# Optimization experiments

Hardware: AMD Instinct MI355X
Metric: run time of the kernel (lower is better)

The kernel has to match this reference:

```python
import jax, jax.numpy as jnp
import numpy as np

N_HEADS = 8
HEAD_D = 64


def setup_inputs() -> dict:
    key = jax.random.key(0)
    ks = jax.random.split(key, 7)
    b, ds, dc = 4, 4096, 256
    ls, lc = 512, 512
    inner = N_HEADS * HEAD_D  # 512
    out_dim = 512
    data = jax.random.normal(ks[0], (b, ds, dc), dtype=jnp.float32)
    latent = jax.random.normal(ks[1], (b, ls, lc), dtype=jnp.float32)
    # torch nn.Linear weights are [out_features, in_features]
    Wq = jax.random.normal(ks[2], (inner, lc), dtype=jnp.float32) * (lc ** -0.5)
    Wk = jax.random.normal(ks[3], (inner, dc), dtype=jnp.float32) * (dc ** -0.5)
    Wv = jax.random.normal(ks[4], (inner, dc), dtype=jnp.float32) * (dc ** -0.5)
    Wo = jax.random.normal(ks[5], (out_dim, inner), dtype=jnp.float32) * (inner ** -0.5)
    bo = jax.random.normal(ks[6], (out_dim,), dtype=jnp.float32) * 0.02
    return {"data": data, "latent": latent, "Wq": Wq, "Wk": Wk, "Wv": Wv, "Wo": Wo, "bo": bo}


def reference(data, latent, Wq, Wk, Wv, Wo, bo):
    b, ds, _ = data.shape
    ls = latent.shape[1]
    scale = HEAD_D ** -0.5
    # projections, split into heads
    Q = (latent @ Wq.T).reshape(b, ls, N_HEADS, HEAD_D)  # [b,ls,h,d]
    K = (data @ Wk.T).reshape(b, ds, N_HEADS, HEAD_D)    # [b,ds,h,d]
    V = (data @ Wv.T).reshape(b, ds, N_HEADS, HEAD_D)
    # logits [b, ds, ls, h]; original broadcasts then sums over head_d -> einsum
    logits = jnp.einsum('blhd,bshd->bslh', Q, K) * scale
    # softmax over key axis (dim 1 = ds), matching attn_logits.softmax(1)
    attn = jax.nn.softmax(logits, axis=1)
    # weighted sum over keys: [b, ls, h, d] -> [b, ls, inner]
    out = jnp.einsum('bshd,bslh->blhd', V, attn).reshape(b, ls, N_HEADS * HEAD_D)
    # output Linear (dropout is identity in eval)
    return out @ Wo.T + bo
```

## Files before the change

kernel.cpp:

```cpp
#include <hip/hip_runtime.h>

typedef __bf16 bf16;
typedef __bf16 bf16x4 __attribute__((ext_vector_type(4)));
typedef __bf16 bf16x8 __attribute__((ext_vector_type(8)));
typedef float  f32x4  __attribute__((ext_vector_type(4)));


__device__ __forceinline__ bf16x8 cvt8(float4 a, float4 b) {
    bf16x8 r;
    r[0] = (bf16)a.x; r[1] = (bf16)a.y; r[2] = (bf16)a.z; r[3] = (bf16)a.w;
    r[4] = (bf16)b.x; r[5] = (bf16)b.y; r[6] = (bf16)b.z; r[7] = (bf16)b.w;
    return r;
}

#define LDT 136
__global__ __launch_bounds__(256) void proj_kvq(
    const float* __restrict__ data, const float* __restrict__ latent,
    const float* __restrict__ Wk, const float* __restrict__ Wv, const float* __restrict__ Wq,
    bf16* __restrict__ K_b, bf16* __restrict__ Vt_b, bf16* __restrict__ Q_b)
{
    __shared__ __align__(16) bf16 arena[128 * LDT];

    const int bx = blockIdx.x;
    const int tid = threadIdx.x;
    const int wave = tid >> 6, lane = tid & 63;
    const int wm = wave >> 1, wn = wave & 1;
    const int l15 = lane & 15, quad = lane >> 4;
    const int rowA = tid >> 2;
    const int c8 = (tid & 3) * 8;

    if (bx >= 64) {
        const int t = bx - 64;
        const int m0 = (t & 127) * 128, n0 = (t >> 7) * 128;
        bf16* As  = arena;
        bf16* Bks = arena + 4096;
        bf16* Bvs = arena + 8192;

        const float* Ar0 = data + (size_t)(m0 + rowA) * 256 + c8;
        const float* Ar1 = Ar0 + 64 * 256;
        const float* Kr0 = Wk + (size_t)(n0 + rowA) * 256 + c8;
        const float* Kr1 = Kr0 + 64 * 256;
        const float* Vr0 = Wv + (size_t)(n0 + rowA) * 256 + c8;
        const float* Vr1 = Vr0 + 64 * 256;

        f32x4 accK[4][4] = {}, accV[4][4] = {};
        float4 a00,a01,a10,a11, k00,k01,k10,k11, v00,v01,v10,v11;

#define LOADF(k) do { \
        a00 = *(const float4*)(Ar0 + (k)); a01 = *(const float4*)(Ar0 + (k) + 4); \
        a10 = *(const float4*)(Ar1 + (k)); a11 = *(const float4*)(Ar1 + (k) + 4); \
        k00 = *(const float4*)(Kr0 + (k)); k01 = *(const float4*)(Kr0 + (k) + 4); \
        k10 = *(const float4*)(Kr1 + (k)); k11 = *(const float4*)(Kr1 + (k) + 4); \
        v00 = *(const float4*)(Vr0 + (k)); v01 = *(const float4*)(Vr0 + (k) + 4); \
        v10 = *(const float4*)(Vr1 + (k)); v11 = *(const float4*)(Vr1 + (k) + 4); \
    } while (0)

        LOADF(0);
        for (int k0 = 0; k0 < 256; k0 += 32) {
            __syncthreads();
            *(bf16x8*)(As + (size_t)tid * 8)         = cvt8(a00, a01);
            *(bf16x8*)(As + 2048 + (size_t)tid * 8)  = cvt8(a10, a11);
            *(bf16x8*)(Bks + (size_t)tid * 8)        = cvt8(k00, k01);
            *(bf16x8*)(Bks + 2048 + (size_t)tid * 8) = cvt8(k10, k11);
            *(bf16x8*)(Bvs + (size_t)tid * 8)        = cvt8(v00, v01);
            *(bf16x8*)(Bvs + 2048 + (size_t)tid * 8) = cvt8(v10, v11);
            if (k0 + 32 < 256) LOADF(k0 + 32);
            __syncthreads();

            bf16x8 af[4];
            #pragma unroll
            for (int mt = 0; mt < 4; mt++)
                af[mt] = *(const bf16x8*)(As + (wm * 64 + mt * 16 + l15) * 32 + quad * 8);
            #pragma unroll
            for (int nt = 0; nt < 4; nt++) {
                bf16x8 bk = *(const bf16x8*)(Bks + (wn * 64 + nt * 16 + l15) * 32 + quad * 8);
                #pragma unroll
                for (int mt = 0; mt < 4; mt++)
                    accK[mt][nt] = __builtin_amdgcn_mfma_f32_16x16x32_bf16(af[mt], bk, accK[mt][nt], 0, 0, 0);
            }
            #pragma unroll
            for (int nt = 0; nt < 4; nt++) {
                bf16x8 bv = *(const bf16x8*)(Bvs + (wn * 64 + nt * 16 + l15) * 32 + quad * 8);
                #pragma unroll
                for (int mt = 0; mt < 4; mt++)
                    accV[mt][nt] = __builtin_amdgcn_mfma_f32_16x16x32_bf16(af[mt], bv, accV[mt][nt], 0, 0, 0);
            }
        }
#undef LOADF

        __syncthreads();
        #pragma unroll
        for (int mt = 0; mt < 4; mt++)
            #pragma unroll
            for (int nt = 0; nt < 4; nt++)
                #pragma unroll
                for (int r = 0; r < 4; r++) {
                    int ml = wm * 64 + mt * 16 + quad * 4 + r;
                    int nl = wn * 64 + nt * 16 + l15;
                    arena[ml * LDT + nl] = (bf16)accK[mt][nt][r];
                }
        __syncthreads();
        #pragma unroll
        for (int c = 0; c < 8; c++) {
            int idx = c * 256 + tid;
            int row = idx >> 4, col = (idx & 15) * 8;
            bf16x8 vv = *(const bf16x8*)(arena + row * LDT + col);
            int m = m0 + row, n = n0 + col;
            *(bf16x8*)(K_b + (size_t)((m >> 12) * 8 + (n >> 6)) * 262144 + (m & 4095) * 64 + (n & 63)) = vv;
        }
        __syncthreads();
        #pragma unroll
        for (int mt = 0; mt < 4; mt++)
            #pragma unroll
            for (int nt = 0; nt < 4; nt++)
                #pragma unroll
                for (int r = 0; r < 4; r++) {
                    int ml = wm * 64 + mt * 16 + quad * 4 + r;
                    int nl = wn * 64 + nt * 16 + l15;
                    arena[nl * LDT + ml] = (bf16)accV[mt][nt][r];
                }
        __syncthreads();
        #pragma unroll
        for (int c = 0; c < 8; c++) {
            int idx = c * 256 + tid;
            int row = idx >> 4, col = (idx & 15) * 8;
            bf16x8 vv = *(const bf16x8*)(arena + row * LDT + col);
            int d = n0 + row, s = m0 + col;
            *(bf16x8*)(Vt_b + (size_t)((s >> 12) * 8 + (d >> 6)) * 262144 + (d & 63) * 4096 + (s & 4095)) = vv;
        }
    } else {
        const int m0 = (bx & 15) * 128, n0 = (bx >> 4) * 128;
        bf16* As = arena;
        bf16* Bs = arena + 4096;

        const float* Ar0 = latent + (size_t)(m0 + rowA) * 512 + c8;
        const float* Ar1 = Ar0 + 64 * 512;
        const float* Br0 = Wq + (size_t)(n0 + rowA) * 512 + c8;
        const float* Br1 = Br0 + 64 * 512;

        f32x4 acc[4][4] = {};
        float4 a00, a01, a10, a11, b00, b01, b10, b11;

#define LOADQ(k) do { \
        a00 = *(const float4*)(Ar0 + (k));  a01 = *(const float4*)(Ar0 + (k) + 4); \
        a10 = *(const float4*)(Ar1 + (k));  a11 = *(const float4*)(Ar1 + (k) + 4); \
        b00 = *(const float4*)(Br0 + (k));  b01 = *(const float4*)(Br0 + (k) + 4); \
        b10 = *(const float4*)(Br1 + (k));  b11 = *(const float4*)(Br1 + (k) + 4); \
    } while (0)

        LOADQ(0);
        for (int k0 = 0; k0 < 512; k0 += 32) {
            __syncthreads();
            *(bf16x8*)(As + (size_t)tid * 8)        = cvt8(a00, a01);
            *(bf16x8*)(As + 2048 + (size_t)tid * 8) = cvt8(a10, a11);
            *(bf16x8*)(Bs + (size_t)tid * 8)        = cvt8(b00, b01);
            *(bf16x8*)(Bs + 2048 + (size_t)tid * 8) = cvt8(b10, b11);
            if (k0 + 32 < 512) LOADQ(k0 + 32);
            __syncthreads();

            bf16x8 af[4], bfr[4];
            #pragma unroll
            for (int mt = 0; mt < 4; mt++)
                af[mt] = *(const bf16x8*)(As + (wm * 64 + mt * 16 + l15) * 32 + quad * 8);
            #pragma unroll
            for (int nt = 0; nt < 4; nt++)
                bfr[nt] = *(const bf16x8*)(Bs + (wn * 64 + nt * 16 + l15) * 32 + quad * 8);
            #pragma unroll
            for (int mt = 0; mt < 4; mt++)
                #pragma unroll
                for (int nt = 0; nt < 4; nt++)
                    acc[mt][nt] = __builtin_amdgcn_mfma_f32_16x16x32_bf16(af[mt], bfr[nt], acc[mt][nt], 0, 0, 0);
        }
#undef LOADQ

        __syncthreads();
        #pragma unroll
        for (int mt = 0; mt < 4; mt++)
            #pragma unroll
            for (int nt = 0; nt < 4; nt++)
                #pragma unroll
                for (int r = 0; r < 4; r++) {
                    int ml = wm * 64 + mt * 16 + quad * 4 + r;
                    int nl = wn * 64 + nt * 16 + l15;
                    arena[ml * LDT + nl] = (bf16)(acc[mt][nt][r] * 0.125f);
                }
        __syncthreads();
        #pragma unroll
        for (int c = 0; c < 8; c++) {
            int idx = c * 256 + tid;
            int row = idx >> 4, col = (idx & 15) * 8;
            bf16x8 vv = *(const bf16x8*)(arena + row * LDT + col);
            int m = m0 + row, n = n0 + col;
            *(bf16x8*)(Q_b + (size_t)((m >> 9) * 8 + (n >> 6)) * 32768 + (m & 511) * 64 + (n & 63)) = vv;
        }
    }
}

#define LDK 72
#define LDP 72
__global__ __launch_bounds__(256) void flash_attn(
    const bf16* __restrict__ Q, const bf16* __restrict__ K,
    const bf16* __restrict__ Vt, float* __restrict__ Opart, float* __restrict__ lbuf)
{
    __shared__ bf16 Ks[64 * LDK];
    __shared__ bf16 Vs[64 * LDK];
    __shared__ bf16 Ps[4][2 * 16 * LDP];

    const int tid = threadIdx.x;
    const int bx = blockIdx.x;
    const int qt = bx >> 7;
    const int bh = (bx & 127) >> 2;
    const int ks = bx & 3;
    const int wave = tid >> 6, lane = tid & 63;
    const int l15 = lane & 15, quad = lane >> 4;

    const bf16* Qb = Q + (size_t)bh * 32768 + (size_t)(qt * 128 + wave * 32 + l15) * 64;
    bf16x8 aq[2][2];
    aq[0][0] = *(const bf16x8*)(Qb + quad * 8);
    aq[0][1] = *(const bf16x8*)(Qb + 32 + quad * 8);
    aq[1][0] = *(const bf16x8*)(Qb + 1024 + quad * 8);
    aq[1][1] = *(const bf16x8*)(Qb + 1024 + 32 + quad * 8);

    const bf16* Kb = K + (size_t)bh * 262144;
    const bf16* Vb = Vt + (size_t)bh * 262144;

    f32x4 oacc[2][4] = {};
    float lsum[2] = {0.f, 0.f};

    const int i0 = tid, i1 = tid + 256;
    const int r0 = i0 >> 3, c0 = (i0 & 7) * 8;
    const int r1 = i1 >> 3, c1 = (i1 & 7) * 8;

    const int kstart = ks * 1024, kend = kstart + 1024;

    uint4 pk0 = *(const uint4*)(Kb + (size_t)(kstart + r0) * 64 + c0);
    uint4 pk1 = *(const uint4*)(Kb + (size_t)(kstart + r1) * 64 + c1);
    uint4 pv0 = *(const uint4*)(Vb + (size_t)r0 * 4096 + kstart + c0);
    uint4 pv1 = *(const uint4*)(Vb + (size_t)r1 * 4096 + kstart + c1);

    bf16* Pw = &Ps[wave][0];

    for (int key0 = kstart; key0 < kend; key0 += 64) {
        __syncthreads();
        *(uint4*)(Ks + r0 * LDK + c0) = pk0;
        *(uint4*)(Ks + r1 * LDK + c1) = pk1;
        *(uint4*)(Vs + r0 * LDK + c0) = pv0;
        *(uint4*)(Vs + r1 * LDK + c1) = pv1;
        if (key0 + 64 < kend) {
            pk0 = *(const uint4*)(Kb + (size_t)(key0 + 64 + r0) * 64 + c0);
            pk1 = *(const uint4*)(Kb + (size_t)(key0 + 64 + r1) * 64 + c1);
            pv0 = *(const uint4*)(Vb + (size_t)r0 * 4096 + key0 + 64 + c0);
            pv1 = *(const uint4*)(Vb + (size_t)r1 * 4096 + key0 + 64 + c1);
        }
        __syncthreads();

        __builtin_amdgcn_s_setprio(1);
        #pragma unroll
        for (int mt = 0; mt < 4; mt++) {
            bf16x8 bk0 = *(const bf16x8*)(Ks + (mt * 16 + l15) * LDK + quad * 8);
            bf16x8 bk1 = *(const bf16x8*)(Ks + (mt * 16 + l15) * LDK + 32 + quad * 8);
            #pragma unroll
            for (int u = 0; u < 2; u++) {
                f32x4 z = {};
                z = __builtin_amdgcn_mfma_f32_16x16x32_bf16(bk0, aq[u][0], z, 0, 0, 0);
                z = __builtin_amdgcn_mfma_f32_16x16x32_bf16(bk1, aq[u][1], z, 0, 0, 0);
                bf16x4 pv4;
                float s = 0.f;
                #pragma unroll
                for (int r = 0; r < 4; r++) {
                    float e = __expf(z[r]);
                    s += e;
                    pv4[r] = (bf16)e;
                }
                lsum[u] += s;
                *(bf16x4*)(Pw + u * 16 * LDP + l15 * LDP + mt * 16 + quad * 4) = pv4;
            }
        }
        __builtin_amdgcn_s_setprio(0);

        bf16x8 ap[2][2];
        #pragma unroll
        for (int u = 0; u < 2; u++) {
            ap[u][0] = *(const bf16x8*)(Pw + u * 16 * LDP + l15 * LDP + quad * 8);
            ap[u][1] = *(const bf16x8*)(Pw + u * 16 * LDP + l15 * LDP + 32 + quad * 8);
        }
        __builtin_amdgcn_s_setprio(1);
        #pragma unroll
        for (int dt = 0; dt < 4; dt++) {
            bf16x8 bv0 = *(const bf16x8*)(Vs + (dt * 16 + l15) * LDK + quad * 8);
            bf16x8 bv1 = *(const bf16x8*)(Vs + (dt * 16 + l15) * LDK + 32 + quad * 8);
            #pragma unroll
            for (int u = 0; u < 2; u++) {
                oacc[u][dt] = __builtin_amdgcn_mfma_f32_16x16x32_bf16(ap[u][0], bv0, oacc[u][dt], 0, 0, 0);
                oacc[u][dt] = __builtin_amdgcn_mfma_f32_16x16x32_bf16(ap[u][1], bv1, oacc[u][dt], 0, 0, 0);
            }
        }
        __builtin_amdgcn_s_setprio(0);
    }

    #pragma unroll
    for (int u = 0; u < 2; u++) {
        lsum[u] += __shfl_xor(lsum[u], 16, 64);
        lsum[u] += __shfl_xor(lsum[u], 32, 64);
    }

    #pragma unroll
    for (int u = 0; u < 2; u++) {
        const int rowbase = bh * 512 + qt * 128 + wave * 32 + u * 16 + quad * 4;
        #pragma unroll
        for (int dt = 0; dt < 4; dt++) {
            #pragma unroll
            for (int r = 0; r < 4; r++) {
                Opart[((size_t)ks * 16384 + rowbase + r) * 64 + dt * 16 + l15] = oacc[u][dt][r];
            }
        }
        if (quad == 0) {
            lbuf[(size_t)ks * 16384 + bh * 512 + qt * 128 + wave * 32 + u * 16 + l15] = lsum[u];
        }
    }
}

__global__ __launch_bounds__(256) void gemm_out(
    const float* __restrict__ Opart, const float* __restrict__ lbuf,
    const float* __restrict__ Wo, const float* __restrict__ bo, float* __restrict__ out)
{
    __shared__ bf16 As[64 * 32];
    __shared__ bf16 Bs[64 * 32];
    const int tid = threadIdx.x;
    const int m0 = blockIdx.x * 64, n0 = blockIdx.y * 64;
    const int wave = tid >> 6, lane = tid & 63;
    const int wm = wave >> 1, wn = wave & 1;
    const int l15 = lane & 15, quad = lane >> 4;
    const int rowA = tid >> 2;
    const int c8 = (tid & 3) * 8;
    const int m = m0 + rowA;
    const int mhi = (m >> 9) << 3, mlo = m & 511;

    f32x4 acc[2][2] = {};
    float4 pa[8]; float pl[4]; float4 pb0, pb1;

    auto loadA = [&](int k0) {
        int kc = k0 + c8;
        int arow = (mhi + (kc >> 6)) * 512 + mlo;
        int d0 = kc & 63;
        #pragma unroll
        for (int ks = 0; ks < 4; ks++) {
            pl[ks] = lbuf[(size_t)ks * 16384 + arow];
            pa[2 * ks]     = *(const float4*)(Opart + ((size_t)ks * 16384 + arow) * 64 + d0);
            pa[2 * ks + 1] = *(const float4*)(Opart + ((size_t)ks * 16384 + arow) * 64 + d0 + 4);
        }
    };
    auto loadB = [&](int k0) {
        pb0 = *(const float4*)(Wo + (size_t)(n0 + rowA) * 512 + k0 + c8);
        pb1 = *(const float4*)(Wo + (size_t)(n0 + rowA) * 512 + k0 + c8 + 4);
    };

    loadA(0); loadB(0);

    for (int k0 = 0; k0 < 512; k0 += 32) {
        __syncthreads();
        {
            float L = pl[0] + pl[1] + pl[2] + pl[3];
            float inv = 1.0f / L;
            float4 s0, s1;
            s0.x = pa[0].x + pa[2].x + pa[4].x + pa[6].x;
            s0.y = pa[0].y + pa[2].y + pa[4].y + pa[6].y;
            s0.z = pa[0].z + pa[2].z + pa[4].z + pa[6].z;
            s0.w = pa[0].w + pa[2].w + pa[4].w + pa[6].w;
            s1.x = pa[1].x + pa[3].x + pa[5].x + pa[7].x;
            s1.y = pa[1].y + pa[3].y + pa[5].y + pa[7].y;
            s1.z = pa[1].z + pa[3].z + pa[5].z + pa[7].z;
            s1.w = pa[1].w + pa[3].w + pa[5].w + pa[7].w;
            s0.x *= inv; s0.y *= inv; s0.z *= inv; s0.w *= inv;
            s1.x *= inv; s1.y *= inv; s1.z *= inv; s1.w *= inv;
            *(bf16x8*)(As + (size_t)tid * 8) = cvt8(s0, s1);
            *(bf16x8*)(Bs + (size_t)tid * 8) = cvt8(pb0, pb1);
        }
        if (k0 + 32 < 512) { loadA(k0 + 32); loadB(k0 + 32); }
        __syncthreads();

        bf16x8 af[2], bfr[2];
        #pragma unroll
        for (int mt = 0; mt < 2; mt++)
            af[mt] = *(const bf16x8*)(As + (wm * 32 + mt * 16 + l15) * 32 + quad * 8);
        #pragma unroll
        for (int nt = 0; nt < 2; nt++)
            bfr[nt] = *(const bf16x8*)(Bs + (wn * 32 + nt * 16 + l15) * 32 + quad * 8);
        #pragma unroll
        for (int mt = 0; mt < 2; mt++)
            #pragma unroll
            for (int nt = 0; nt < 2; nt++)
                acc[mt][nt] = __builtin_amdgcn_mfma_f32_16x16x32_bf16(af[mt], bfr[nt], acc[mt][nt], 0, 0, 0);
    }

    #pragma unroll
    for (int mt = 0; mt < 2; mt++) {
        #pragma unroll
        for (int nt = 0; nt < 2; nt++) {
            #pragma unroll
            for (int r = 0; r < 4; r++) {
                int mm = m0 + wm * 32 + mt * 16 + quad * 4 + r;
                int nn = n0 + wn * 32 + nt * 16 + l15;
                out[(size_t)mm * 512 + nn] = acc[mt][nt][r] + bo[nn];
            }
        }
    }
}

extern "C" void kernel_launch(void* const* d_in, const int* in_sizes, int n_in,
                              void* d_out, int out_size, void* d_ws, size_t ws_size,
                              hipStream_t stream) {
    const float* data   = (const float*)d_in[0];
    const float* latent = (const float*)d_in[1];
    const float* Wq = (const float*)d_in[2];
    const float* Wk = (const float*)d_in[3];
    const float* Wv = (const float*)d_in[4];
    const float* Wo = (const float*)d_in[5];
    const float* bo = (const float*)d_in[6];
    float* out = (float*)d_out;

    bf16* ws = (bf16*)d_ws;
    bf16* Q_b    = ws;
    bf16* K_b    = Q_b + 1048576;
    bf16* Vt_b   = K_b + 8388608;
    float* Opart = (float*)(Vt_b + 8388608);
    float* lbuf  = Opart + 4 * 16384 * 64;

    proj_kvq<<<576, 256, 0, stream>>>(data, latent, Wk, Wv, Wq, K_b, Vt_b, Q_b);
    flash_attn<<<512, 256, 0, stream>>>(Q_b, K_b, Vt_b, Opart, lbuf);
    gemm_out<<<dim3(32, 8), 256, 0, stream>>>(Opart, lbuf, Wo, bo, out);
}
```

Before: 149.1 us.

## Pre-convert inputs to bf16, use async global-to-LDS loads, split merge from output GEMM

Adds a kernel that converts data, latent and all weights to bf16 up front, folding the attention scale into Wq. The projection kernel then stages bf16 tiles through double-buffered direct global-to-LDS loads instead of register fp32 loads and conversion. The split-K merge of partial attention outputs moves out of the output GEMM into its own kernel that writes bf16 O. This removes redundant fp32 reloads and conversions inside the GEMMs, in exchange for two extra launches and an extra read and write pass over the data.

```diff
diff --git a/kernel.cpp b/kernel.cpp
--- a/kernel.cpp
+++ b/kernel.cpp
@@ -13,82 +13,102 @@
     return r;
 }
 
+__device__ __forceinline__ void gload16(const bf16* g, bf16* l) {
+    __builtin_amdgcn_global_load_lds(
+        (const __attribute__((address_space(1))) unsigned int*)(g),
+        (__attribute__((address_space(3))) unsigned int*)(l), 16, 0, 0);
+}
+
+__global__ __launch_bounds__(256) void cvt_in(
+    const float* __restrict__ data, const float* __restrict__ latent,
+    const float* __restrict__ Wq, const float* __restrict__ Wk,
+    const float* __restrict__ Wv, const float* __restrict__ Wo,
+    bf16* __restrict__ db, bf16* __restrict__ lb, bf16* __restrict__ qb,
+    bf16* __restrict__ kb, bf16* __restrict__ vb, bf16* __restrict__ ob)
+{
+    const int bx = blockIdx.x;
+    const float* src; bf16* dst; float scale = 1.0f; int base;
+    if      (bx < 2048) { src = data;   dst = db; base = bx; }
+    else if (bx < 2560) { src = latent; dst = lb; base = bx - 2048; }
+    else if (bx < 2688) { src = Wq;     dst = qb; base = bx - 2560; scale = 0.125f; }
+    else if (bx < 2752) { src = Wk;     dst = kb; base = bx - 2688; }
+    else if (bx < 2816) { src = Wv;     dst = vb; base = bx - 2752; }
+    else                { src = Wo;     dst = ob; base = bx - 2816; }
+    size_t off = (size_t)base * 2048 + (size_t)threadIdx.x * 8;
+    float4 a = *(const float4*)(src + off);
+    float4 b = *(const float4*)(src + off + 4);
+    a.x *= scale; a.y *= scale; a.z *= scale; a.w *= scale;
+    b.x *= scale; b.y *= scale; b.z *= scale; b.w *= scale;
+    *(bf16x8*)(dst + off) = cvt8(a, b);
+}
+
 #define LDT 136
 __global__ __launch_bounds__(256) void proj_kvq(
-    const float* __restrict__ data, const float* __restrict__ latent,
-    const float* __restrict__ Wk, const float* __restrict__ Wv, const float* __restrict__ Wq,
+    const bf16* __restrict__ data, const bf16* __restrict__ latent,
+    const bf16* __restrict__ Wk, const bf16* __restrict__ Wv, const bf16* __restrict__ Wq,
     bf16* __restrict__ K_b, bf16* __restrict__ Vt_b, bf16* __restrict__ Q_b)
 {
-    __shared__ __align__(16) bf16 arena[128 * LDT];
+    __shared__ __align__(16) bf16 arena[24576];
 
     const int bx = blockIdx.x;
     const int tid = threadIdx.x;
     const int wave = tid >> 6, lane = tid & 63;
     const int wm = wave >> 1, wn = wave & 1;
     const int l15 = lane & 15, quad = lane >> 4;
-    const int rowA = tid >> 2;
-    const int c8 = (tid & 3) * 8;
+    const int rowS = wave * 32 + (lane >> 2);
+    const int colS = (lane & 3) * 8;
 
     if (bx >= 64) {
         const int t = bx - 64;
         const int m0 = (t & 127) * 128, n0 = (t >> 7) * 128;
-        bf16* As  = arena;
-        bf16* Bks = arena + 4096;
-        bf16* Bvs = arena + 8192;
-
-        const float* Ar0 = data + (size_t)(m0 + rowA) * 256 + c8;
-        const float* Ar1 = Ar0 + 64 * 256;
-        const float* Kr0 = Wk + (size_t)(n0 + rowA) * 256 + c8;
-        const float* Kr1 = Kr0 + 64 * 256;
-        const float* Vr0 = Wv + (size_t)(n0 + rowA) * 256 + c8;
-        const float* Vr1 = Vr0 + 64 * 256;
+
+        const bf16* Asrc = data + (size_t)(m0 + rowS) * 256 + colS;
+        const bf16* Ksrc = Wk   + (size_t)(n0 + rowS) * 256 + colS;
+        const bf16* Vsrc = Wv   + (size_t)(n0 + rowS) * 256 + colS;
 
         f32x4 accK[4][4] = {}, accV[4][4] = {};
-        float4 a00,a01,a10,a11, k00,k01,k10,k11, v00,v01,v10,v11;
-
-#define LOADF(k) do { \
-        a00 = *(const float4*)(Ar0 + (k)); a01 = *(const float4*)(Ar0 + (k) + 4); \
-        a10 = *(const float4*)(Ar1 + (k)); a11 = *(const float4*)(Ar1 + (k) + 4); \
-        k00 = *(const float4*)(Kr0 + (k)); k01 = *(const float4*)(Kr0 + (k) + 4); \
-        k10 = *(const float4*)(Kr1 + (k)); k11 = *(const float4*)(Kr1 + (k) + 4); \
-        v00 = *(const float4*)(Vr0 + (k)); v01 = *(const float4*)(Vr0 + (k) + 4); \
-        v10 = *(const float4*)(Vr1 + (k)); v11 = *(const float4*)(Vr1 + (k) + 4); \
+
+#define STAGE_KV(buf, k0) do { \
+        bf16* Lb = arena + (buf) * 12288 + wave * 1024; \
+        gload16(Asrc + (k0),        Lb);          \
+        gload16(Asrc + (k0) + 4096, Lb + 512);    \
+        gload16(Ksrc + (k0),        Lb + 4096);   \
+        gload16(Ksrc + (k0) + 4096, Lb + 4608);   \
+        gload16(Vsrc + (k0),        Lb + 8192);   \
+        gload16(Vsrc + (k0) + 4096, Lb + 8704);   \
     } while (0)
 
-        LOADF(0);
+        STAGE_KV(0, 0);
+        asm volatile("s_waitcnt vmcnt(0)" ::: "memory");
+        __syncthreads();
+        int cur = 0;
         for (int k0 = 0; k0 < 256; k0 += 32) {
-            __syncthreads();
-            *(bf16x8*)(As + (size_t)tid * 8)         = cvt8(a00, a01);
-            *(bf16x8*)(As + 2048 + (size_t)tid * 8)  = cvt8(a10, a11);
-            *(bf16x8*)(Bks + (size_t)tid * 8)        = cvt8(k00, k01);
-            *(bf16x8*)(Bks + 2048 + (size_t)tid * 8) = cvt8(k10, k11);
-            *(bf16x8*)(Bvs + (size_t)tid * 8)        = cvt8(v00, v01);
-            *(bf16x8*)(Bvs + 2048 + (size_t)tid * 8) = cvt8(v10, v11);
-            if (k0 + 32 < 256) LOADF(k0 + 32);
-            __syncthreads();
+            if (k0 + 32 < 256) STAGE_KV(cur ^ 1, k0 + 32);
+            const bf16* B = arena + cur * 12288;
 
             bf16x8 af[4];
             #pragma unroll
             for (int mt = 0; mt < 4; mt++)
-                af[mt] = *(const bf16x8*)(As + (wm * 64 + mt * 16 + l15) * 32 + quad * 8);
+                af[mt] = *(const bf16x8*)(B + (wm * 64 + mt * 16 + l15) * 32 + quad * 8);
             #pragma unroll
             for (int nt = 0; nt < 4; nt++) {
-                bf16x8 bk = *(const bf16x8*)(Bks + (wn * 64 + nt * 16 + l15) * 32 + quad * 8);
+                bf16x8 bk = *(const bf16x8*)(B + 4096 + (wn * 64 + nt * 16 + l15) * 32 + quad * 8);
                 #pragma unroll
                 for (int mt = 0; mt < 4; mt++)
                     accK[mt][nt] = __builtin_amdgcn_mfma_f32_16x16x32_bf16(af[mt], bk, accK[mt][nt], 0, 0, 0);
             }
             #pragma unroll
             for (int nt = 0; nt < 4; nt++) {
-                bf16x8 bv = *(const bf16x8*)(Bvs + (wn * 64 + nt * 16 + l15) * 32 + quad * 8);
+                bf16x8 bv = *(const bf16x8*)(B + 8192 + (wn * 64 + nt * 16 + l15) * 32 + quad * 8);
                 #pragma unroll
                 for (int mt = 0; mt < 4; mt++)
                     accV[mt][nt] = __builtin_amdgcn_mfma_f32_16x16x32_bf16(af[mt], bv, accV[mt][nt], 0, 0, 0);
             }
-        }
-#undef LOADF
-
-        __syncthreads();
+            __syncthreads();
+            cur ^= 1;
+        }
+#undef STAGE_KV
+
         #pragma unroll
         for (int mt = 0; mt < 4; mt++)
             #pragma unroll
@@ -130,50 +150,45 @@
         }
     } else {
         const int m0 = (bx & 15) * 128, n0 = (bx >> 4) * 128;
-        bf16* As = arena;
-        bf16* Bs = arena + 4096;
-
-        const float* Ar0 = latent + (size_t)(m0 + rowA) * 512 + c8;
-        const float* Ar1 = Ar0 + 64 * 512;
-        const float* Br0 = Wq + (size_t)(n0 + rowA) * 512 + c8;
-        const float* Br1 = Br0 + 64 * 512;
+
+        const bf16* Asrc = latent + (size_t)(m0 + rowS) * 512 + colS;
+        const bf16* Bsrc = Wq     + (size_t)(n0 + rowS) * 512 + colS;
 
         f32x4 acc[4][4] = {};
-        float4 a00, a01, a10, a11, b00, b01, b10, b11;
-
-#define LOADQ(k) do { \
-        a00 = *(const float4*)(Ar0 + (k));  a01 = *(const float4*)(Ar0 + (k) + 4); \
-        a10 = *(const float4*)(Ar1 + (k));  a11 = *(const float4*)(Ar1 + (k) + 4); \
-        b00 = *(const float4*)(Br0 + (k));  b01 = *(const float4*)(Br0 + (k) + 4); \
-        b10 = *(const float4*)(Br1 + (k));  b11 = *(const float4*)(Br1 + (k) + 4); \
+
+#define STAGE_Q(buf, k0) do { \
+        bf16* Lb = arena + (buf) * 8192 + wave * 1024; \
+        gload16(Asrc + (k0),        Lb);          \
+        gload16(Asrc + (k0) + 8192, Lb + 512);    \
+        gload16(Bsrc + (k0),        Lb + 4096);   \
+        gload16(Bsrc + (k0) + 8192, Lb + 4608);   \
     } while (0)
 
-        LOADQ(0);
+        STAGE_Q(0, 0);
+        asm volatile("s_waitcnt vmcnt(0)" ::: "memory");
+        __syncthreads();
+        int cur = 0;
         for (int k0 = 0; k0 < 512; k0 += 32) {
-            __syncthreads();
-            *(bf16x8*)(As + (size_t)tid * 8)        = cvt8(a00, a01);
-            *(bf16x8*)(As + 2048 + (size_t)tid * 8) = cvt8(a10, a11);
-            *(bf16x8*)(Bs + (size_t)tid * 8)        = cvt8(b00, b01);
-            *(bf16x8*)(Bs + 2048 + (size_t)tid * 8) = cvt8(b10, b11);
-            if (k0 + 32 < 512) LOADQ(k0 + 32);
-            __syncthreads();
+            if (k0 + 32 < 512) STAGE_Q(cur ^ 1, k0 + 32);
+            const bf16* B = arena + cur * 8192;
 
             bf16x8 af[4], bfr[4];
             #pragma unroll
             for (int mt = 0; mt < 4; mt++)
-                af[mt] = *(const bf16x8*)(As + (wm * 64 + mt * 16 + l15) * 32 + quad * 8);
+                af[mt] = *(const bf16x8*)(B + (wm * 64 + mt * 16 + l15) * 32 + quad * 8);
             #pragma unroll
             for (int nt = 0; nt < 4; nt++)
-                bfr[nt] = *(const bf16x8*)(Bs + (wn * 64 + nt * 16 + l15) * 32 + quad * 8);
+                bfr[nt] = *(const bf16x8*)(B + 4096 + (wn * 64 + nt * 16 + l15) * 32 + quad * 8);
             #pragma unroll
             for (int mt = 0; mt < 4; mt++)
                 #pragma unroll
                 for (int nt = 0; nt < 4; nt++)
                     acc[mt][nt] = __builtin_amdgcn_mfma_f32_16x16x32_bf16(af[mt], bfr[nt], acc[mt][nt], 0, 0, 0);
-        }
-#undef LOADQ
-
-        __syncthreads();
+            __syncthreads();
+            cur ^= 1;
+        }
+#undef STAGE_Q
+
         #pragma unroll
         for (int mt = 0; mt < 4; mt++)
             #pragma unroll
@@ -182,7 +197,7 @@
                 for (int r = 0; r < 4; r++) {
                     int ml = wm * 64 + mt * 16 + quad * 4 + r;
                     int nl = wn * 64 + nt * 16 + l15;
-                    arena[ml * LDT + nl] = (bf16)(acc[mt][nt][r] * 0.125f);
+                    arena[ml * LDT + nl] = (bf16)acc[mt][nt][r];
                 }
         __syncthreads();
         #pragma unroll
@@ -320,12 +335,36 @@
     }
 }
 
+__global__ __launch_bounds__(256) void merge_o(
+    const float* __restrict__ Opart, const float* __restrict__ lbuf, bf16* __restrict__ O)
+{
+    const int idx = blockIdx.x * 256 + threadIdx.x;
+    const int row = idx >> 3;
+    const int d0 = (idx & 7) * 8;
+    float L = 0.f;
+    float4 s0 = {0,0,0,0}, s1 = {0,0,0,0};
+    #pragma unroll
+    for (int ks = 0; ks < 4; ks++) {
+        L += lbuf[(size_t)ks * 16384 + row];
+        float4 p0 = *(const float4*)(Opart + ((size_t)ks * 16384 + row) * 64 + d0);
+        float4 p1 = *(const float4*)(Opart + ((size_t)ks * 16384 + row) * 64 + d0 + 4);
+        s0.x += p0.x; s0.y += p0.y; s0.z += p0.z; s0.w += p0.w;
+        s1.x += p1.x; s1.y += p1.y; s1.z += p1.z; s1.w += p1.w;
+    }
+    float inv = 1.0f / L;
+    s0.x *= inv; s0.y *= inv; s0.z *= inv; s0.w *= inv;
+    s1.x *= inv; s1.y *= inv; s1.z *= inv; s1.w *= inv;
+    const int bh = row >> 9, l = row & 511;
+    const int b = bh >> 3, h = bh & 7;
+    *(bf16x8*)(O + ((size_t)(b * 512 + l)) * 512 + h * 64 + d0) = cvt8(s0, s1);
+}
+
 __global__ __launch_bounds__(256) void gemm_out(
-    const float* __restrict__ Opart, const float* __restrict__ lbuf,
-    const float* __restrict__ Wo, const float* __restrict__ bo, float* __restrict__ out)
+    const bf16* __restrict__ O, const bf16* __restrict__ Wo_b,
+    const float* __restrict__ bo, float* __restrict__ out)
 {
-    __shared__ bf16 As[64 * 32];
-    __shared__ bf16 Bs[64 * 32];
+    __shared__ bf16 As[2048];
+    __shared__ bf16 Bs[2048];
     const int tid = threadIdx.x;
     const int m0 = blockIdx.x * 64, n0 = blockIdx.y * 64;
     const int wave = tid >> 6, lane = tid & 63;
@@ -333,50 +372,19 @@
     const int l15 = lane & 15, quad = lane >> 4;
     const int rowA = tid >> 2;
     const int c8 = (tid & 3) * 8;
-    const int m = m0 + rowA;
-    const int mhi = (m >> 9) << 3, mlo = m & 511;
 
     f32x4 acc[2][2] = {};
-    float4 pa[8]; float pl[4]; float4 pb0, pb1;
-
-    auto loadA = [&](int k0) {
-        int kc = k0 + c8;
-        int arow = (mhi + (kc >> 6)) * 512 + mlo;
-        int d0 = kc & 63;
-        #pragma unroll
-        for (int ks = 0; ks < 4; ks++) {
-            pl[ks] = lbuf[(size_t)ks * 16384 + arow];
-            pa[2 * ks]     = *(const float4*)(Opart + ((size_t)ks * 16384 + arow) * 64 + d0);
-            pa[2 * ks + 1] = *(const float4*)(Opart + ((size_t)ks * 16384 + arow) * 64 + d0 + 4);
-        }
-    };
-    auto loadB = [&](int k0) {
-        pb0 = *(const float4*)(Wo + (size_t)(n0 + rowA) * 512 + k0 + c8);
-        pb1 = *(const float4*)(Wo + (size_t)(n0 + rowA) * 512 + k0 + c8 + 4);
-    };
-
-    loadA(0); loadB(0);
+    bf16x8 pa = *(const bf16x8*)(O    + (size_t)(m0 + rowA) * 512 + c8);
+    bf16x8 pb = *(const bf16x8*)(Wo_b + (size_t)(n0 + rowA) * 512 + c8);
 
     for (int k0 = 0; k0 < 512; k0 += 32) {
         __syncthreads();
-        {
-            float L = pl[0] + pl[1] + pl[2] + pl[3];
-            float inv = 1.0f / L;
-            float4 s0, s1;
-            s0.x = pa[0].x + pa[2].x + pa[4].x + pa[6].x;
-            s0.y = pa[0].y + pa[2].y + pa[4].y + pa[6].y;
-            s0.z = pa[0].z + pa[2].z + pa[4].z + pa[6].z;
-            s0.w = pa[0].w + pa[2].w + pa[4].w + pa[6].w;
-            s1.x = pa[1].x + pa[3].x + pa[5].x + pa[7].x;
-            s1.y = pa[1].y + pa[3].y + pa[5].y + pa[7].y;
-            s1.z = pa[1].z + pa[3].z + pa[5].z + pa[7].z;
-            s1.w = pa[1].w + pa[3].w + pa[5].w + pa[7].w;
-            s0.x *= inv; s0.y *= inv; s0.z *= inv; s0.w *= inv;
-            s1.x *= inv; s1.y *= inv; s1.z *= inv; s1.w *= inv;
-            *(bf16x8*)(As + (size_t)tid * 8) = cvt8(s0, s1);
-            *(bf16x8*)(Bs + (size_t)tid * 8) = cvt8(pb0, pb1);
-        }
-        if (k0 + 32 < 512) { loadA(k0 + 32); loadB(k0 + 32); }
+        *(bf16x8*)(As + (size_t)tid * 8) = pa;
+        *(bf16x8*)(Bs + (size_t)tid * 8) = pb;
+        if (k0 + 32 < 512) {
+            pa = *(const bf16x8*)(O    + (size_t)(m0 + rowA) * 512 + k0 + 32 + c8);
+            pb = *(const bf16x8*)(Wo_b + (size_t)(n0 + rowA) * 512 + k0 + 32 + c8);
+        }
         __syncthreads();
 
         bf16x8 af[2], bfr[2];
@@ -425,8 +433,18 @@
     bf16* Vt_b   = K_b + 8388608;
     float* Opart = (float*)(Vt_b + 8388608);
     float* lbuf  = Opart + 4 * 16384 * 64;
-
-    proj_kvq<<<576, 256, 0, stream>>>(data, latent, Wk, Wv, Wq, K_b, Vt_b, Q_b);
+    bf16* data_bf = (bf16*)(lbuf + 4 * 16384);
+    bf16* lat_bf  = data_bf + 4194304;
+    bf16* Wq_bf   = lat_bf + 1048576;
+    bf16* Wk_bf   = Wq_bf + 262144;
+    bf16* Wv_bf   = Wk_bf + 131072;
+    bf16* Wo_bf   = Wv_bf + 131072;
+    bf16* O_bf    = Wo_bf + 262144;
+
+    cvt_in<<<2944, 256, 0, stream>>>(data, latent, Wq, Wk, Wv, Wo,
+                                     data_bf, lat_bf, Wq_bf, Wk_bf, Wv_bf, Wo_bf);
+    proj_kvq<<<576, 256, 0, stream>>>(data_bf, lat_bf, Wk_bf, Wv_bf, Wq_bf, K_b, Vt_b, Q_b);
     flash_attn<<<512, 256, 0, stream>>>(Q_b, K_b, Vt_b, Opart, lbuf);
-    gemm_out<<<dim3(32, 8), 256, 0, stream>>>(Opart, lbuf, Wo, bo, out);
-}
+    merge_o<<<512, 256, 0, stream>>>(Opart, lbuf, O_bf);
+    gemm_out<<<dim3(32, 8), 256, 0, stream>>>(O_bf, Wo_bf, bo, out);
+}
```

Result: faster. 135.2 us (-9.3%).
